# Kernel tuning notes

Hardware: AMD Instinct MI355X
Metric: run time of the kernel (lower is better)

Reference implementation:

```python
import jax, jax.numpy as jnp
import numpy as np

N = 100000      # nodes
E = 1200000     # edges (avg degree ~12)
F_IN = 64       # input feature dim
HID = 64        # hidden_channels
OUT = 64        # out_channels


def setup_inputs() -> dict:
    key = jax.random.key(0)
    ks = jax.random.split(key, 9)
    s_in = 1.0 / np.sqrt(F_IN)
    s_h = 1.0 / np.sqrt(HID)
    inp = {
        "x": jax.random.normal(ks[0], (N, F_IN), dtype=jnp.float32),
        "edge_index": jax.random.randint(ks[1], (2, E), 0, N, dtype=jnp.int64),
        # conv_in: lin_l (with bias) applied to aggregated msgs, lin_r (no bias) to self
        "Wl_in": jax.random.normal(ks[2], (HID, F_IN), dtype=jnp.float32) * s_in,
        "bl_in": jnp.zeros((HID,), dtype=jnp.float32),
        "Wr_in": jax.random.normal(ks[3], (HID, F_IN), dtype=jnp.float32) * s_in,
        # conv_med (shared across the 2 middle applications)
        "Wl_med": jax.random.normal(ks[4], (HID, HID), dtype=jnp.float32) * s_h,
        "bl_med": jnp.zeros((HID,), dtype=jnp.float32),
        "Wr_med": jax.random.normal(ks[5], (HID, HID), dtype=jnp.float32) * s_h,
        # conv_out
        "Wl_out": jax.random.normal(ks[6], (OUT, HID), dtype=jnp.float32) * s_h,
        "bl_out": jnp.zeros((OUT,), dtype=jnp.float32),
        "Wr_out": jax.random.normal(ks[7], (OUT, HID), dtype=jnp.float32) * s_h,
    }
    return inp


def reference(x, edge_index, Wl_in, bl_in, Wr_in, Wl_med, bl_med, Wr_med,
              Wl_out, bl_out, Wr_out):
    src = edge_index[0]
    dst = edge_index[1]
    n = x.shape[0]

    def sage(h, Wl, bl, Wr):
        # sum-aggregate neighbor messages h_j into each destination node i
        agg = jax.ops.segment_sum(h[src], dst, num_segments=n)  # [N, F]
        return agg @ Wl.T + bl + h @ Wr.T

    # eval mode: dropout is identity
    h = jnp.tanh(sage(x, Wl_in, bl_in, Wr_in))
    for _ in range(2):  # conv_med applied twice with shared weights
        h = jnp.tanh(sage(h, Wl_med, bl_med, Wr_med))
    return sage(h, Wl_out, bl_out, Wr_out)
```

## Files before the change

### kernel.cpp

```cpp
#include <hip/hip_runtime.h>
#include <cstdint>

#define F 64
#define TILE1 8192
#define MAXFB 1024
#define SCAN_BLK 1024

typedef short bf16x8 __attribute__((ext_vector_type(8)));
typedef float f32x4  __attribute__((ext_vector_type(4)));

__device__ __forceinline__ unsigned short f2b(float f) {
    unsigned u = __float_as_uint(f);
    unsigned r = u + 0x7fffu + ((u >> 16) & 1u);
    return (unsigned short)(r >> 16);
}
__device__ __forceinline__ void add8(float* a, uint4 u) {
    const unsigned* p = (const unsigned*)&u;
#pragma unroll
    for (int i = 0; i < 4; ++i) {
        a[2 * i + 0] += __uint_as_float(p[i] << 16);
        a[2 * i + 1] += __uint_as_float(p[i] & 0xffff0000u);
    }
}

__global__ __launch_bounds__(256) void hist_kernel(
    const int* __restrict__ dst, int* __restrict__ binMat,
    int E, int NB1, int nf) {
    __shared__ int h[MAXFB];
    int t = threadIdx.x;
    for (int i = t; i < nf; i += 256) h[i] = 0;
    __syncthreads();
    int base = blockIdx.x * TILE1;
    int end = min(base + TILE1, E);
    const int4* d4 = (const int4*)dst;
    int n4 = (end - base) >> 2;
    int b4 = base >> 2;
    for (int k = t; k < n4; k += 256) {
        int4 v = d4[b4 + k];
        atomicAdd(&h[v.x >> 7], 1);
        atomicAdd(&h[v.y >> 7], 1);
        atomicAdd(&h[v.z >> 7], 1);
        atomicAdd(&h[v.w >> 7], 1);
    }
    __syncthreads();
    for (int i = t; i < nf; i += 256) binMat[i * NB1 + blockIdx.x] = h[i];
}

__global__ __launch_bounds__(SCAN_BLK) void scan_blocks_kernel(
    int* __restrict__ a, int* __restrict__ blockSums, int len) {
    __shared__ int sh[SCAN_BLK];
    int t = threadIdx.x;
    int i = blockIdx.x * SCAN_BLK + t;
    int v = (i < len) ? a[i] : 0;
    sh[t] = v;
    __syncthreads();
    for (int off = 1; off < SCAN_BLK; off <<= 1) {
        int add = (t >= off) ? sh[t - off] : 0;
        __syncthreads();
        sh[t] += add;
        __syncthreads();
    }
    int incl = sh[t];
    if (i < len) a[i] = incl - v;
    if (t == SCAN_BLK - 1) blockSums[blockIdx.x] = incl;
}

__global__ __launch_bounds__(SCAN_BLK) void scan_sums_kernel(
    int* __restrict__ blockSums, int nb) {
    __shared__ int sh[SCAN_BLK];
    int t = threadIdx.x;
    int v = (t < nb) ? blockSums[t] : 0;
    sh[t] = v;
    __syncthreads();
    for (int off = 1; off < SCAN_BLK; off <<= 1) {
        int add = (t >= off) ? sh[t - off] : 0;
        __syncthreads();
        sh[t] += add;
        __syncthreads();
    }
    if (t < nb) blockSums[t] = sh[t] - v;
}

__global__ __launch_bounds__(256) void scan_add_kernel(
    int* __restrict__ a, const int* __restrict__ blockSums, int len) {
    int i = blockIdx.x * 256 + threadIdx.x;
    if (i < len) a[i] += blockSums[i >> 10];
}

__global__ __launch_bounds__(256) void scatter_kernel(
    const int* __restrict__ src, const int* __restrict__ dst,
    const int* __restrict__ binMat, unsigned* __restrict__ stage2,
    int E, int NB1, int nf) {
    __shared__ int cur[MAXFB];
    int t = threadIdx.x;
    for (int i = t; i < nf; i += 256) cur[i] = binMat[i * NB1 + blockIdx.x];
    __syncthreads();
    int base = blockIdx.x * TILE1;
    int end = min(base + TILE1, E);
    const int4* s4 = (const int4*)src;
    const int4* d4 = (const int4*)dst;
    int n4 = (end - base) >> 2;
    int b4 = base >> 2;
    for (int k = t; k < n4; k += 256) {
        int4 s = s4[b4 + k];
        int4 d = d4[b4 + k];
        int p0 = atomicAdd(&cur[d.x >> 7], 1);
        int p1 = atomicAdd(&cur[d.y >> 7], 1);
        int p2 = atomicAdd(&cur[d.z >> 7], 1);
        int p3 = atomicAdd(&cur[d.w >> 7], 1);
        stage2[p0] = ((unsigned)(d.x & 127) << 17) | (unsigned)s.x;
        stage2[p1] = ((unsigned)(d.y & 127) << 17) | (unsigned)s.y;
        stage2[p2] = ((unsigned)(d.z & 127) << 17) | (unsigned)s.z;
        stage2[p3] = ((unsigned)(d.w & 127) << 17) | (unsigned)s.w;
    }
}

__global__ __launch_bounds__(256) void phase2_kernel(
    const unsigned* __restrict__ stage2, const int* __restrict__ binMat,
    int* __restrict__ csrSrc, int* __restrict__ rowStart,
    int E, int NB1, int nf) {
    __shared__ int cnt[128];
    __shared__ int pre[129];
    __shared__ int cur[128];
    int b = blockIdx.x;
    int t = threadIdx.x;
    int s = binMat[b * NB1];
    int e2 = (b + 1 < nf) ? binMat[(b + 1) * NB1] : E;
    if (t < 128) cnt[t] = 0;
    __syncthreads();
    for (int i = s + t; i < e2; i += 256)
        atomicAdd(&cnt[(stage2[i] >> 17) & 127], 1);
    __syncthreads();
    if (t < 128) pre[t + 1] = cnt[t];
    if (t == 0) pre[0] = 0;
    __syncthreads();
    for (int off = 1; off < 128; off <<= 1) {
        int v = 0;
        if (t < 128 && (t + 1) > off) v = pre[t + 1 - off];
        __syncthreads();
        if (t < 128 && (t + 1) > off) pre[t + 1] += v;
        __syncthreads();
    }
    if (t < 128) cur[t] = pre[t];
    if (t < 129) rowStart[b * 128 + t] = s + pre[t];
    __syncthreads();
    for (int i = s + t; i < e2; i += 256) {
        unsigned w = stage2[i];
        int pos = atomicAdd(&cur[(w >> 17) & 127], 1);
        csrSrc[s + pos] = (int)(w & 0x1FFFFu);
    }
}

__global__ __launch_bounds__(256) void prep_kernel(
    const float* __restrict__ Wl0, const float* __restrict__ Wr0,
    const float* __restrict__ Wl1, const float* __restrict__ Wr1,
    const float* __restrict__ Wl2, const float* __restrict__ Wr2,
    ushort* __restrict__ wbuf,
    const float* __restrict__ x, ushort* __restrict__ xb, int nElem) {
    int b = blockIdx.x;
    int t = threadIdx.x;
    if (b < 12) {
        int g = b * 256 + t;
        int set = g >> 10;
        int fl = g & 1023;
        int f = fl >> 6;
        int l = fl & 63;
        int s = f >> 2;
        int ot = f & 3;
        const float* Wl = (set == 0) ? Wl0 : (set == 1) ? Wl1 : Wl2;
        const float* Wr = (set == 0) ? Wr0 : (set == 1) ? Wr1 : Wr2;
        int o = ot * 16 + (l & 15);
        int k0 = s * 32 + (l >> 4) * 8;
        unsigned d[4];
#pragma unroll
        for (int p = 0; p < 4; ++p) {
            int ka = k0 + 2 * p, kb = k0 + 2 * p + 1;
            float va = (ka < 64) ? Wl[o * 64 + ka] : Wr[o * 64 + (ka - 64)];
            float vb = (kb < 64) ? Wl[o * 64 + kb] : Wr[o * 64 + (kb - 64)];
            d[p] = (unsigned)f2b(va) | ((unsigned)f2b(vb) << 16);
        }
        ((uint4*)wbuf)[g] = make_uint4(d[0], d[1], d[2], d[3]);
    } else {
        int i = (b - 12) * 256 + t;
        int n4 = nElem >> 2;
        if (i < n4) {
            float4 v = ((const float4*)x)[i];
            uint2 o;
            o.x = (unsigned)f2b(v.x) | ((unsigned)f2b(v.y) << 16);
            o.y = (unsigned)f2b(v.z) | ((unsigned)f2b(v.w) << 16);
            ((uint2*)xb)[i] = o;
        }
    }
}

__global__ __launch_bounds__(256, 8) void gather_kernel(
    const ushort* __restrict__ hb, const int* __restrict__ rowStart,
    const int* __restrict__ csrSrc, ushort* __restrict__ aggB, int nr) {
    int gid = blockIdx.x * 256 + threadIdx.x;
    int node = gid >> 3;
    int c = gid & 7;
    if (node >= nr) return;

    const uint4* h16 = (const uint4*)hb;
    float a[8] = {0.f, 0.f, 0.f, 0.f, 0.f, 0.f, 0.f, 0.f};

    int e = rowStart[node];
    int end = rowStart[node + 1];
    for (; e + 3 < end; e += 4) {
        int s0 = csrSrc[e + 0];
        int s1 = csrSrc[e + 1];
        int s2 = csrSrc[e + 2];
        int s3 = csrSrc[e + 3];
        uint4 u0 = h16[(size_t)s0 * 8 + c];
        uint4 u1 = h16[(size_t)s1 * 8 + c];
        uint4 u2 = h16[(size_t)s2 * 8 + c];
        uint4 u3 = h16[(size_t)s3 * 8 + c];
        add8(a, u0); add8(a, u1); add8(a, u2); add8(a, u3);
    }
    for (; e < end; ++e) {
        uint4 u0 = h16[(size_t)csrSrc[e] * 8 + c];
        add8(a, u0);
    }

    unsigned d[4];
#pragma unroll
    for (int p = 0; p < 4; ++p)
        d[p] = (unsigned)f2b(a[2 * p]) | ((unsigned)f2b(a[2 * p + 1]) << 16);
    ((uint4*)aggB)[(size_t)node * 8 + c] = make_uint4(d[0], d[1], d[2], d[3]);
}

__global__ __launch_bounds__(256, 4) void matvec_mfma(
    const ushort* __restrict__ aggB, const ushort* __restrict__ hb,
    const ushort* __restrict__ wbuf, const float* __restrict__ bl,
    void* __restrict__ out, int n, int flags) {
    __shared__ float outT[128 * 68];

    int t = threadIdx.x;
    int w = t >> 6;
    int l = t & 63;
    int quad = l >> 4;
    int lo = l & 15;
    int node0 = blockIdx.x * 128 + w * 32;

    f32x4 acc[2][4];
#pragma unroll
    for (int ot = 0; ot < 4; ++ot) {
        float bv = bl[ot * 16 + lo];
        f32x4 bvv = {bv, bv, bv, bv};
        acc[0][ot] = bvv;
        acc[1][ot] = bvv;
    }

#pragma unroll
    for (int s = 0; s < 4; ++s) {
        const ushort* hbase = (s < 2) ? aggB : hb;
        bf16x8 A[2];
#pragma unroll
        for (int mt = 0; mt < 2; ++mt) {
            size_t node = (size_t)node0 + mt * 16 + lo;
            A[mt] = *(const bf16x8*)(hbase + node * 64 + (s & 1) * 32 + quad * 8);
        }
#pragma unroll
        for (int ot = 0; ot < 4; ++ot) {
            bf16x8 B = *(const bf16x8*)(wbuf + (((s * 4 + ot) * 64) + l) * 8);
#pragma unroll
            for (int mt = 0; mt < 2; ++mt)
                acc[mt][ot] = __builtin_amdgcn_mfma_f32_16x16x32_bf16(
                    A[mt], B, acc[mt][ot], 0, 0, 0);
        }
    }

#pragma unroll
    for (int mt = 0; mt < 2; ++mt) {
#pragma unroll
        for (int ot = 0; ot < 4; ++ot) {
            f32x4 v = acc[mt][ot];
            if (flags & 1) {
                v[0] = tanhf(v[0]); v[1] = tanhf(v[1]);
                v[2] = tanhf(v[2]); v[3] = tanhf(v[3]);
            }
            int row = w * 32 + mt * 16 + quad * 4;
            int col = ot * 16 + lo;
#pragma unroll
            for (int r = 0; r < 4; ++r)
                outT[(row + r) * 68 + col] = v[r];
        }
    }

    int row = w * 32 + (l >> 1);
    int node = blockIdx.x * 128 + row;
    if (node < n) {
        const float* srcp = &outT[row * 68 + (l & 1) * 32];
        if (flags & 2) {
            uint4* o8 = (uint4*)out;
#pragma unroll
            for (int q = 0; q < 4; ++q) {
                unsigned d[4];
#pragma unroll
                for (int p = 0; p < 4; ++p) {
                    float va = srcp[q * 8 + 2 * p];
                    float vb = srcp[q * 8 + 2 * p + 1];
                    d[p] = (unsigned)f2b(va) | ((unsigned)f2b(vb) << 16);
                }
                o8[(size_t)node * 8 + (l & 1) * 4 + q] = make_uint4(d[0], d[1], d[2], d[3]);
            }
        } else {
            float4* o16 = (float4*)out;
#pragma unroll
            for (int q = 0; q < 8; ++q) {
                float4 v = *(const float4*)(srcp + q * 4);
                o16[(size_t)node * 16 + (l & 1) * 8 + q] = v;
            }
        }
    }
}

extern "C" void kernel_launch(void* const* d_in, const int* in_sizes, int n_in,
                              void* d_out, int out_size, void* d_ws, size_t ws_size,
                              hipStream_t stream) {
    const float* x      = (const float*)d_in[0];
    const int*   edges  = (const int*)d_in[1];
    const float* Wl_in  = (const float*)d_in[2];
    const float* bl_in  = (const float*)d_in[3];
    const float* Wr_in  = (const float*)d_in[4];
    const float* Wl_med = (const float*)d_in[5];
    const float* bl_med = (const float*)d_in[6];
    const float* Wr_med = (const float*)d_in[7];
    const float* Wl_out = (const float*)d_in[8];
    const float* bl_out = (const float*)d_in[9];
    const float* Wr_out = (const float*)d_in[10];

    const int N = in_sizes[0] / F;
    const int E = in_sizes[1] / 2;
    const int* src = edges;
    const int* dst = edges + E;

    const int nf  = (N + 127) >> 7;
    const int NB1 = (E + TILE1 - 1) / TILE1;
    const int NR  = nf * 128;
    const int scanLen = nf * NB1;
    const int nbScan = (scanLen + SCAN_BLK - 1) / SCAN_BLK;

    ushort*  wbuf      = (ushort*)d_ws;
    ushort*  aggB      = wbuf + 3 * 8192;
    ushort*  xb        = aggB + (size_t)NR * F;
    ushort*  hAb       = xb + (size_t)NR * F;
    ushort*  hBb       = hAb + (size_t)NR * F;
    int*     rowStart  = (int*)(hBb + (size_t)NR * F);
    int*     blockSums = rowStart + NR + 2;
    int*     binMat    = blockSums + SCAN_BLK;
    unsigned* stage2   = (unsigned*)(binMat + scanLen);
    int*     csrSrc    = (int*)(stage2 + E);

    const int gather_blocks = NR / 32;
    const int prep_blocks = 12 + (N * F / 4 + 255) / 256;

    prep_kernel<<<prep_blocks, 256, 0, stream>>>(Wl_in, Wr_in, Wl_med, Wr_med,
                                                 Wl_out, Wr_out, wbuf, x, xb, N * F);

    hist_kernel<<<NB1, 256, 0, stream>>>(dst, binMat, E, NB1, nf);
    scan_blocks_kernel<<<nbScan, SCAN_BLK, 0, stream>>>(binMat, blockSums, scanLen);
    scan_sums_kernel<<<1, SCAN_BLK, 0, stream>>>(blockSums, nbScan);
    scan_add_kernel<<<(scanLen + 255) / 256, 256, 0, stream>>>(binMat, blockSums, scanLen);
    scatter_kernel<<<NB1, 256, 0, stream>>>(src, dst, binMat, stage2, E, NB1, nf);
    phase2_kernel<<<nf, 256, 0, stream>>>(stage2, binMat, csrSrc, rowStart, E, NB1, nf);

    gather_kernel<<<gather_blocks, 256, 0, stream>>>(xb, rowStart, csrSrc, aggB, NR);
    matvec_mfma<<<nf, 256, 0, stream>>>(aggB, xb, wbuf + 0,     bl_in,  hAb,   N, 3);
    gather_kernel<<<gather_blocks, 256, 0, stream>>>(hAb, rowStart, csrSrc, aggB, NR);
    matvec_mfma<<<nf, 256, 0, stream>>>(aggB, hAb, wbuf + 8192, bl_med, hBb,   N, 3);
    gather_kernel<<<gather_blocks, 256, 0, stream>>>(hBb, rowStart, csrSrc, aggB, NR);
    matvec_mfma<<<nf, 256, 0, stream>>>(aggB, hBb, wbuf + 8192, bl_med, hAb,   N, 3);
    gather_kernel<<<gather_blocks, 256, 0, stream>>>(hAb, rowStart, csrSrc, aggB, NR);
    matvec_mfma<<<nf, 256, 0, stream>>>(aggB, hAb, wbuf + 16384, bl_out, d_out, N, 0);
}
```

Before: 292.6 us.

## Fuse neighbor gather into MFMA layer kernel via shared-memory staging

```diff
diff --git a/kernel.cpp b/kernel.cpp
--- a/kernel.cpp
+++ b/kernel.cpp
@@ -193,54 +193,54 @@
     }
 }
 
-__global__ __launch_bounds__(256, 8) void gather_kernel(
+__global__ __launch_bounds__(256, 4) void fused_layer(
     const ushort* __restrict__ hb, const int* __restrict__ rowStart,
-    const int* __restrict__ csrSrc, ushort* __restrict__ aggB, int nr) {
-    int gid = blockIdx.x * 256 + threadIdx.x;
-    int node = gid >> 3;
-    int c = gid & 7;
-    if (node >= nr) return;
-
+    const int* __restrict__ csrSrc, const ushort* __restrict__ wbuf,
+    const float* __restrict__ bl, void* __restrict__ out, int n, int flags) {
+    __shared__ __align__(16) ushort smem[128 * 72];
+
+    int t = threadIdx.x;
+    int node0b = blockIdx.x * 128;
     const uint4* h16 = (const uint4*)hb;
-    float a[8] = {0.f, 0.f, 0.f, 0.f, 0.f, 0.f, 0.f, 0.f};
-
-    int e = rowStart[node];
-    int end = rowStart[node + 1];
-    for (; e + 3 < end; e += 4) {
-        int s0 = csrSrc[e + 0];
-        int s1 = csrSrc[e + 1];
-        int s2 = csrSrc[e + 2];
-        int s3 = csrSrc[e + 3];
-        uint4 u0 = h16[(size_t)s0 * 8 + c];
-        uint4 u1 = h16[(size_t)s1 * 8 + c];
-        uint4 u2 = h16[(size_t)s2 * 8 + c];
-        uint4 u3 = h16[(size_t)s3 * 8 + c];
-        add8(a, u0); add8(a, u1); add8(a, u2); add8(a, u3);
-    }
-    for (; e < end; ++e) {
-        uint4 u0 = h16[(size_t)csrSrc[e] * 8 + c];
-        add8(a, u0);
-    }
-
-    unsigned d[4];
-#pragma unroll
-    for (int p = 0; p < 4; ++p)
-        d[p] = (unsigned)f2b(a[2 * p]) | ((unsigned)f2b(a[2 * p + 1]) << 16);
-    ((uint4*)aggB)[(size_t)node * 8 + c] = make_uint4(d[0], d[1], d[2], d[3]);
-}
-
-__global__ __launch_bounds__(256, 4) void matvec_mfma(
-    const ushort* __restrict__ aggB, const ushort* __restrict__ hb,
-    const ushort* __restrict__ wbuf, const float* __restrict__ bl,
-    void* __restrict__ out, int n, int flags) {
-    __shared__ float outT[128 * 68];
-
-    int t = threadIdx.x;
+
+    {
+        int c = t & 7;
+        int nlb = t >> 3;
+#pragma unroll 1
+        for (int r = 0; r < 4; ++r) {
+            int nl = r * 32 + nlb;
+            int node = node0b + nl;
+            float a[8] = {0.f, 0.f, 0.f, 0.f, 0.f, 0.f, 0.f, 0.f};
+            int e = rowStart[node];
+            int end = rowStart[node + 1];
+            for (; e + 3 < end; e += 4) {
+                int s0 = csrSrc[e + 0];
+                int s1 = csrSrc[e + 1];
+                int s2 = csrSrc[e + 2];
+                int s3 = csrSrc[e + 3];
+                uint4 u0 = h16[(size_t)s0 * 8 + c];
+                uint4 u1 = h16[(size_t)s1 * 8 + c];
+                uint4 u2 = h16[(size_t)s2 * 8 + c];
+                uint4 u3 = h16[(size_t)s3 * 8 + c];
+                add8(a, u0); add8(a, u1); add8(a, u2); add8(a, u3);
+            }
+            for (; e < end; ++e) {
+                uint4 u0 = h16[(size_t)csrSrc[e] * 8 + c];
+                add8(a, u0);
+            }
+            unsigned d[4];
+#pragma unroll
+            for (int p = 0; p < 4; ++p)
+                d[p] = (unsigned)f2b(a[2 * p]) | ((unsigned)f2b(a[2 * p + 1]) << 16);
+            *(uint4*)(smem + nl * 72 + c * 8) = make_uint4(d[0], d[1], d[2], d[3]);
+        }
+    }
+    __syncthreads();
+
     int w = t >> 6;
     int l = t & 63;
     int quad = l >> 4;
     int lo = l & 15;
-    int node0 = blockIdx.x * 128 + w * 32;
 
     f32x4 acc[2][4];
 #pragma unroll
@@ -253,12 +253,16 @@
 
 #pragma unroll
     for (int s = 0; s < 4; ++s) {
-        const ushort* hbase = (s < 2) ? aggB : hb;
         bf16x8 A[2];
 #pragma unroll
         for (int mt = 0; mt < 2; ++mt) {
-            size_t node = (size_t)node0 + mt * 16 + lo;
-            A[mt] = *(const bf16x8*)(hbase + node * 64 + (s & 1) * 32 + quad * 8);
+            if (s < 2) {
+                int nl = w * 32 + mt * 16 + lo;
+                A[mt] = *(const bf16x8*)(smem + nl * 72 + s * 32 + quad * 8);
+            } else {
+                size_t node = (size_t)node0b + w * 32 + mt * 16 + lo;
+                A[mt] = *(const bf16x8*)(hb + node * 64 + (s & 1) * 32 + quad * 8);
+            }
         }
 #pragma unroll
         for (int ot = 0; ot < 4; ++ot) {
@@ -269,49 +273,61 @@
                     A[mt], B, acc[mt][ot], 0, 0, 0);
         }
     }
-
-#pragma unroll
-    for (int mt = 0; mt < 2; ++mt) {
-#pragma unroll
-        for (int ot = 0; ot < 4; ++ot) {
-            f32x4 v = acc[mt][ot];
-            if (flags & 1) {
-                v[0] = tanhf(v[0]); v[1] = tanhf(v[1]);
-                v[2] = tanhf(v[2]); v[3] = tanhf(v[3]);
-            }
-            int row = w * 32 + mt * 16 + quad * 4;
-            int col = ot * 16 + lo;
-#pragma unroll
-            for (int r = 0; r < 4; ++r)
-                outT[(row + r) * 68 + col] = v[r];
-        }
-    }
-
-    int row = w * 32 + (l >> 1);
-    int node = blockIdx.x * 128 + row;
-    if (node < n) {
-        const float* srcp = &outT[row * 68 + (l & 1) * 32];
-        if (flags & 2) {
-            uint4* o8 = (uint4*)out;
-#pragma unroll
-            for (int q = 0; q < 4; ++q) {
-                unsigned d[4];
-#pragma unroll
-                for (int p = 0; p < 4; ++p) {
-                    float va = srcp[q * 8 + 2 * p];
-                    float vb = srcp[q * 8 + 2 * p + 1];
-                    d[p] = (unsigned)f2b(va) | ((unsigned)f2b(vb) << 16);
+    __syncthreads();
+
+    float* outT = (float*)smem;
+    int whalf = w >> 1;
+    int wrow = (w & 1) * 32;
+
+#pragma unroll
+    for (int half = 0; half < 2; ++half) {
+        if (whalf == half) {
+#pragma unroll
+            for (int mt = 0; mt < 2; ++mt) {
+#pragma unroll
+                for (int ot = 0; ot < 4; ++ot) {
+                    f32x4 v = acc[mt][ot];
+                    if (flags & 1) {
+                        v[0] = tanhf(v[0]); v[1] = tanhf(v[1]);
+                        v[2] = tanhf(v[2]); v[3] = tanhf(v[3]);
+                    }
+                    int row = wrow + mt * 16 + quad * 4;
+                    int col = ot * 16 + lo;
+#pragma unroll
+                    for (int r = 0; r < 4; ++r)
+                        outT[(row + r) * 68 + col] = v[r];
                 }
-                o8[(size_t)node * 8 + (l & 1) * 4 + q] = make_uint4(d[0], d[1], d[2], d[3]);
-            }
-        } else {
-            float4* o16 = (float4*)out;
-#pragma unroll
-            for (int q = 0; q < 8; ++q) {
-                float4 v = *(const float4*)(srcp + q * 4);
-                o16[(size_t)node * 16 + (l & 1) * 8 + q] = v;
-            }
-        }
+            }
+        }
+        __syncthreads();
+        int hr = t >> 2;
+        int node = node0b + half * 64 + hr;
+        if (node < n) {
+            const float* srcp = &outT[hr * 68 + (t & 3) * 16];
+            if (flags & 2) {
+                uint4* o8 = (uint4*)out;
+#pragma unroll
+                for (int q = 0; q < 2; ++q) {
+                    unsigned dd[4];
+#pragma unroll
+                    for (int p = 0; p < 4; ++p) {
+                        float va = srcp[q * 8 + 2 * p];
+                        float vb = srcp[q * 8 + 2 * p + 1];
+                        dd[p] = (unsigned)f2b(va) | ((unsigned)f2b(vb) << 16);
+                    }
+                    o8[(size_t)node * 8 + (t & 3) * 2 + q] =
+                        make_uint4(dd[0], dd[1], dd[2], dd[3]);
+                }
+            } else {
+                float4* o16 = (float4*)out;
+#pragma unroll
+                for (int q = 0; q < 4; ++q) {
+                    float4 v = *(const float4*)(srcp + q * 4);
+                    o16[(size_t)node * 16 + (t & 3) * 4 + q] = v;
+                }
+            }
+        }
+        if (half == 0) __syncthreads();
     }
 }
 
@@ -342,8 +358,7 @@
     const int nbScan = (scanLen + SCAN_BLK - 1) / SCAN_BLK;
 
     ushort*  wbuf      = (ushort*)d_ws;
-    ushort*  aggB      = wbuf + 3 * 8192;
-    ushort*  xb        = aggB + (size_t)NR * F;
+    ushort*  xb        = wbuf + 3 * 8192;
     ushort*  hAb       = xb + (size_t)NR * F;
     ushort*  hBb       = hAb + (size_t)NR * F;
     int*     rowStart  = (int*)(hBb + (size_t)NR * F);
@@ -352,7 +367,6 @@
     unsigned* stage2   = (unsigned*)(binMat + scanLen);
     int*     csrSrc    = (int*)(stage2 + E);
 
-    const int gather_blocks = NR / 32;
     const int prep_blocks = 12 + (N * F / 4 + 255) / 256;
 
     prep_kernel<<<prep_blocks, 256, 0, stream>>>(Wl_in, Wr_in, Wl_med, Wr_med,
@@ -365,12 +379,8 @@
     scatter_kernel<<<NB1, 256, 0, stream>>>(src, dst, binMat, stage2, E, NB1, nf);
     phase2_kernel<<<nf, 256, 0, stream>>>(stage2, binMat, csrSrc, rowStart, E, NB1, nf);
 
-    gather_kernel<<<gather_blocks, 256, 0, stream>>>(xb, rowStart, csrSrc, aggB, NR);
-    matvec_mfma<<<nf, 256, 0, stream>>>(aggB, xb, wbuf + 0,     bl_in,  hAb,   N, 3);
-    gather_kernel<<<gather_blocks, 256, 0, stream>>>(hAb, rowStart, csrSrc, aggB, NR);
-    matvec_mfma<<<nf, 256, 0, stream>>>(aggB, hAb, wbuf + 8192, bl_med, hBb,   N, 3);
-    gather_kernel<<<gather_blocks, 256, 0, stream>>>(hBb, rowStart, csrSrc, aggB, NR);
-    matvec_mfma<<<nf, 256, 0, stream>>>(aggB, hBb, wbuf + 8192, bl_med, hAb,   N, 3);
-    gather_kernel<<<gather_blocks, 256, 0, stream>>>(hAb, rowStart, csrSrc, aggB, NR);
-    matvec_mfma<<<nf, 256, 0, stream>>>(aggB, hAb, wbuf + 16384, bl_out, d_out, N, 0);
-}
+    fused_layer<<<nf, 256, 0, stream>>>(xb,  rowStart, csrSrc, wbuf,         bl_in,  hAb,   N, 3);
+    fused_layer<<<nf, 256, 0, stream>>>(hAb, rowStart, csrSrc, wbuf + 8192,  bl_med, hBb,   N, 3);
+    fused_layer<<<nf, 256, 0, stream>>>(hBb, rowStart, csrSrc, wbuf + 8192,  bl_med, hAb,   N, 3);
+    fused_layer<<<nf, 256, 0, stream>>>(hAb, rowStart, csrSrc, wbuf + 16384, bl_out, d_out, N, 0);
+}
```

New measurement: 297.0 us. About the same (+1.5%).
